# Kernel tuning notes

Hardware: AMD Instinct MI355X
Metric: run time of the kernel (lower is better)

Reference implementation:

```python
import jax, jax.numpy as jnp
import numpy as np

N = 50000   # atoms
E = 800000  # edges (avg degree 16)
F = 128     # n_atombasis
K = 64      # n_radialbasis
NRI = 3     # residual layers in interaction
NRA = 2     # atomic residual layers


def ssp(x):
    # PhysNet shifted softplus: softplus(x) - log(2)
    return jax.nn.softplus(x) - jnp.asarray(np.log(2.0), x.dtype)


def setup_inputs() -> dict:
    key = jax.random.key(0)
    ks = jax.random.split(key, 24)
    s = 0.05  # small weight scale (orig xavier gain=1e-4; nonzero so math is non-degenerate)
    inp = {
        "features": jax.random.normal(ks[0], (N, F), jnp.float32),
        "descriptors": jax.random.normal(ks[1], (E, K), jnp.float32),
        "idx_i": jnp.sort(jax.random.randint(ks[2], (E,), 0, N)),
        "idx_j": jax.random.randint(ks[3], (E,), 0, N),
        "Wdesc": jax.random.normal(ks[4], (F, K), jnp.float32) * s,   # desc2feat, no bias
        "Wi": jax.random.normal(ks[5], (F, F), jnp.float32) * s,
        "bi": jnp.zeros((F,), jnp.float32),
        "Wj": jax.random.normal(ks[6], (F, F), jnp.float32) * s,
        "bj": jnp.zeros((F,), jnp.float32),
        "Wri1": jax.random.normal(ks[7], (NRI, F, F), jnp.float32) * s,
        "bri1": jnp.zeros((NRI, F), jnp.float32),
        "Wri2": jax.random.normal(ks[8], (NRI, F, F), jnp.float32) * s,
        "bri2": jnp.zeros((NRI, F), jnp.float32),
        "Wd": jax.random.normal(ks[9], (F, F), jnp.float32) * s,
        "bd": jnp.zeros((F,), jnp.float32),
        "u": jnp.ones((F,), jnp.float32),
        "Wra1": jax.random.normal(ks[10], (NRA, F, F), jnp.float32) * s,
        "bra1": jnp.zeros((NRA, F), jnp.float32),
        "Wra2": jax.random.normal(ks[11], (NRA, F, F), jnp.float32) * s,
        "bra2": jnp.zeros((NRA, F), jnp.float32),
    }
    return inp


def _residual(m, W1, b1, W2, b2):
    # ResidualLayer (eval mode, no dropout): m + residual(dense(act(m)))
    y = ssp(m)
    h = ssp(y @ W1.T + b1)  # dense (with activation)
    return m + h @ W2.T + b2  # residual (no activation)


def reference(features, descriptors, Wdesc, Wi, bi, Wj, bj,
              Wri1, bri1, Wri2, bri2, Wd, bd, u,
              Wra1, bra1, Wra2, bra2, idx_i, idx_j):
    x = features                               # [N, F]
    xa = ssp(x)
    g = descriptors @ Wdesc.T                  # [E, F] edge gate
    xi = ssp(xa @ Wi.T + bi)                   # [N, F]
    xj_all = ssp(xa @ Wj.T + bj)               # [N, F]
    pxj = g * xj_all[idx_j]                    # gather -> elementwise mul, [E, F]
    xj = jax.ops.segment_sum(pxj, idx_i, num_segments=x.shape[0])  # scatter-add [N, F]
    message = xi + xj
    for k in range(NRI):
        message = _residual(message, Wri1[k], bri1[k], Wri2[k], bri2[k])
    message = ssp(message)
    x = u * x + message @ Wd.T + bd
    for k in range(NRA):
        x = _residual(x, Wra1[k], bra1[k], Wra2[k], bra2[k])
    return x
```

## Files before the change

### kernel.cpp

```cpp
#include <hip/hip_runtime.h>
#include <math.h>

#define NA 50000
#define NE 800000
#define FDIM 128
#define KDIM 64
#define NRI 3
#define NRA 2
#define ETILES 10

typedef unsigned short ushort_t;
typedef unsigned int uint_t;
typedef __attribute__((ext_vector_type(8))) short short8v;
typedef __attribute__((ext_vector_type(4))) float f32x4;
typedef __attribute__((ext_vector_type(4))) unsigned short u16x4;

__device__ __forceinline__ float ssp_f(float x) {
    float e = __expf(-fabsf(x));
    return fmaxf(x, 0.0f) + __logf(1.0f + e) - 0.69314718055994530942f;
}
__device__ __forceinline__ ushort_t f2bf(float x) {
    unsigned u = __float_as_uint(x);
    u += 0x7FFFu + ((u >> 16) & 1u);
    return (ushort_t)(u >> 16);
}
__device__ __forceinline__ float bf2f(ushort_t h) {
    return __uint_as_float(((unsigned)h) << 16);
}
__device__ __forceinline__ f32x4 ssp4(f32x4 v) {
    f32x4 r;
    #pragma unroll
    for (int j = 0; j < 4; ++j) r[j] = ssp_f(v[j]);
    return r;
}
__device__ __forceinline__ u16x4 pack4(f32x4 v) {
    u16x4 p;
    #pragma unroll
    for (int j = 0; j < 4; ++j) p[j] = f2bf(v[j]);
    return p;
}

__global__ __launch_bounds__(256) void k_wconv(
    const float* __restrict__ Wdesc, const float* __restrict__ Wi,
    const float* __restrict__ Wj,    const float* __restrict__ Wri1,
    const float* __restrict__ Wri2,  const float* __restrict__ Wd,
    const float* __restrict__ Wra1,  const float* __restrict__ Wra2,
    ushort_t* __restrict__ wbf)
{
    const int seg = blockIdx.y;
    const int idx = blockIdx.x * 2048 + threadIdx.x * 8;
    const float* s; ushort_t* d; int cnt;
    const int CH = 40960;
    switch (seg) {
    case 0: cnt = 8192;  if (idx >= cnt) return; s = Wdesc + idx; d = wbf + idx; break;
    case 1: cnt = 16384; if (idx >= cnt) return; s = Wi + idx;    d = wbf + 8192 + idx; break;
    case 2: cnt = 16384; if (idx >= cnt) return; s = Wj + idx;    d = wbf + 24576 + idx; break;
    case 3: { cnt = 3*16384; if (idx >= cnt) return; int k = idx/16384, o = idx - k*16384;
              s = Wri1 + idx; d = wbf + CH + (2*k)*16384 + o; break; }
    case 4: { cnt = 3*16384; if (idx >= cnt) return; int k = idx/16384, o = idx - k*16384;
              s = Wri2 + idx; d = wbf + CH + (2*k+1)*16384 + o; break; }
    case 5: cnt = 16384; if (idx >= cnt) return; s = Wd + idx; d = wbf + CH + 6*16384 + idx; break;
    case 6: { cnt = 2*16384; if (idx >= cnt) return; int k = idx/16384, o = idx - k*16384;
              s = Wra1 + idx; d = wbf + CH + (7+2*k)*16384 + o; break; }
    default:{ cnt = 2*16384; if (idx >= cnt) return; int k = idx/16384, o = idx - k*16384;
              s = Wra2 + idx; d = wbf + CH + (8+2*k)*16384 + o; break; }
    }
    #pragma unroll
    for (int j = 0; j < 8; ++j) d[j] = f2bf(s[j]);
}

__device__ __forceinline__ void stage_w(const ushort_t* __restrict__ src,
                                        ushort_t (*wlds)[136], int t)
{
    const int r = t >> 1, c0 = (t & 1) * 64;
    const short8v* s = (const short8v*)(src + (size_t)r * FDIM + c0);
    #pragma unroll
    for (int q = 0; q < 8; ++q)
        *(short8v*)&wlds[r][c0 + q * 8] = s[q];
}

__device__ __forceinline__ void gemm_tile_T(
    const ushort_t (*actA)[136], const ushort_t (*wlds)[136],
    int w, int lrow, int kgrp, const float* __restrict__ bias, f32x4 acc[8])
{
    short8v bfr[4];
    #pragma unroll
    for (int ks = 0; ks < 4; ++ks)
        bfr[ks] = *(const short8v*)&actA[16 * w + lrow][ks * 32 + kgrp * 8];
    #pragma unroll
    for (int nf = 0; nf < 8; ++nf)
        acc[nf] = *(const f32x4*)(bias + 16 * nf + 4 * kgrp);
    #pragma unroll
    for (int nf = 0; nf < 8; ++nf)
        #pragma unroll
        for (int ks = 0; ks < 4; ++ks) {
            short8v av = *(const short8v*)&wlds[16 * nf + lrow][ks * 32 + kgrp * 8];
            acc[nf] = __builtin_amdgcn_mfma_f32_16x16x32_bf16(av, bfr[ks], acc[nf], 0, 0, 0);
        }
}

__device__ __forceinline__ void write_act_T(
    ushort_t (*actA)[136], int w, int lrow, int kgrp, const f32x4 v[8])
{
    #pragma unroll
    for (int nf = 0; nf < 8; ++nf)
        *(u16x4*)&actA[16 * w + lrow][16 * nf + 4 * kgrp] = pack4(ssp4(v[nf]));
}

__global__ __launch_bounds__(256) void k_node_pre(
    const float* __restrict__ feat, const ushort_t* __restrict__ wbf,
    const float* __restrict__ bi, const float* __restrict__ bj,
    float* __restrict__ xi_out, ushort_t* __restrict__ xja_out)
{
    __shared__ ushort_t actA[64][136];
    __shared__ ushort_t wlds[128][136];
    const int t = threadIdx.x, lane = t & 63, w = t >> 6;
    const int lrow = lane & 15, kgrp = lane >> 4;
    const int atom = blockIdx.x * 64 + 16 * w + lrow;
    const bool ok = atom < NA;

    f32x4 v[8];
    #pragma unroll
    for (int nf = 0; nf < 8; ++nf)
        v[nf] = ok ? *(const f32x4*)(feat + (size_t)atom * FDIM + 16 * nf + 4 * kgrp)
                   : (f32x4){0.f, 0.f, 0.f, 0.f};
    write_act_T(actA, w, lrow, kgrp, v);
    __syncthreads();
    stage_w(wbf + 8192, wlds, t);
    __syncthreads();
    f32x4 acc[8];
    gemm_tile_T(actA, wlds, w, lrow, kgrp, bi, acc);
    if (ok)
        #pragma unroll
        for (int nf = 0; nf < 8; ++nf)
            *(f32x4*)(xi_out + (size_t)atom * FDIM + 16 * nf + 4 * kgrp) = ssp4(acc[nf]);
    __syncthreads();
    stage_w(wbf + 24576, wlds, t);
    __syncthreads();
    gemm_tile_T(actA, wlds, w, lrow, kgrp, bj, acc);
    if (ok)
        #pragma unroll
        for (int nf = 0; nf < 8; ++nf)
            *(u16x4*)(xja_out + (size_t)atom * FDIM + 16 * nf + 4 * kgrp) = pack4(ssp4(acc[nf]));
}

__device__ __forceinline__ short8v pack8(const float* p) {
    short8v r;
    #pragma unroll
    for (int j = 0; j < 8; ++j) r[j] = (short)f2bf(p[j]);
    return r;
}

__global__ __launch_bounds__(256) void k_edge_fused(
    const float* __restrict__ desc, const ushort_t* __restrict__ wdbf,
    const int* __restrict__ idx_i, const int* __restrict__ idx_j,
    const ushort_t* __restrict__ xja,
    float* __restrict__ msg)
{
    __shared__ ushort_t pl[64][136];
    __shared__ int ii[64];
    const int t = threadIdx.x, lane = t & 63, w = t >> 6;
    const int lrow = lane & 15, kgrp = lane >> 4;
    const int ebase = blockIdx.x * (64 * ETILES);
    const int eoff = w * 16 + lrow;

    short8v a[8][2];
    #pragma unroll
    for (int nf = 0; nf < 8; ++nf)
        #pragma unroll
        for (int ks = 0; ks < 2; ++ks)
            a[nf][ks] = *(const short8v*)(wdbf + (size_t)(16 * nf + lrow) * KDIM
                                          + ks * 32 + kgrp * 8);

    int er = ebase + eoff;
    int jj = idx_j[er];
    float t0[8], t1[8];
    {
        const float* q = desc + (size_t)er * KDIM + kgrp * 8;
        *(float4*)(t0)     = *(const float4*)q;
        *(float4*)(t0 + 4) = *(const float4*)(q + 4);
        *(float4*)(t1)     = *(const float4*)(q + 32);
        *(float4*)(t1 + 4) = *(const float4*)(q + 36);
    }

    for (int tt = 0; tt < ETILES; ++tt) {
        if (t < 64) ii[t] = idx_i[ebase + tt * 64 + t];

        short8v b0 = pack8(t0), b1 = pack8(t1);
        f32x4 acc[8];
        #pragma unroll
        for (int nf = 0; nf < 8; ++nf) acc[nf] = (f32x4){0.f, 0.f, 0.f, 0.f};
        #pragma unroll
        for (int nf = 0; nf < 8; ++nf) {
            acc[nf] = __builtin_amdgcn_mfma_f32_16x16x32_bf16(a[nf][0], b0, acc[nf], 0,0,0);
            acc[nf] = __builtin_amdgcn_mfma_f32_16x16x32_bf16(a[nf][1], b1, acc[nf], 0,0,0);
        }

        #pragma unroll
        for (int nf = 0; nf < 8; ++nf) {
            u16x4 xv = *(const u16x4*)(xja + (size_t)jj * FDIM + 16 * nf + 4 * kgrp);
            f32x4 pr;
            #pragma unroll
            for (int j = 0; j < 4; ++j) pr[j] = acc[nf][j] * bf2f(xv[j]);
            *(u16x4*)&pl[w * 16 + lrow][16 * nf + 4 * kgrp] = pack4(pr);
        }

        if (tt + 1 < ETILES) {
            er += 64;
            jj = idx_j[er];
            const float* q = desc + (size_t)er * KDIM + kgrp * 8;
            *(float4*)(t0)     = *(const float4*)q;
            *(float4*)(t0 + 4) = *(const float4*)(q + 4);
            *(float4*)(t1)     = *(const float4*)(q + 32);
            *(float4*)(t1 + 4) = *(const float4*)(q + 36);
        }

        __syncthreads();

        const int f = t & 127, h = t >> 7;
        const int r0 = h * 32;
        float s = 0.0f;
        int cur = ii[r0];
        #pragma unroll
        for (int g = 0; g < 8; ++g) {
            float v[4];
            int id[4];
            #pragma unroll
            for (int qq = 0; qq < 4; ++qq) {
                v[qq]  = bf2f(pl[r0 + g * 4 + qq][f]);
                id[qq] = ii[r0 + g * 4 + qq];
            }
            #pragma unroll
            for (int qq = 0; qq < 4; ++qq) {
                if (id[qq] != cur) {
                    unsafeAtomicAdd(&msg[(size_t)cur * FDIM + f], s);
                    s = 0.0f; cur = id[qq];
                }
                s += v[qq];
            }
        }
        unsafeAtomicAdd(&msg[(size_t)cur * FDIM + f], s);

        __syncthreads();
    }
}

__global__ __launch_bounds__(256) void k_chain(
    const float* __restrict__ msgp, const float* __restrict__ feat,
    const float* __restrict__ u, const ushort_t* __restrict__ wch,
    const float* __restrict__ bri1, const float* __restrict__ bri2,
    const float* __restrict__ bd,
    const float* __restrict__ bra1, const float* __restrict__ bra2,
    float* __restrict__ xout)
{
    __shared__ ushort_t actA[64][136];
    __shared__ ushort_t wlds[128][136];
    const int t = threadIdx.x, lane = t & 63, w = t >> 6;
    const int lrow = lane & 15, kgrp = lane >> 4;
    const int atom = blockIdx.x * 64 + 16 * w + lrow;
    const bool ok = atom < NA;

    f32x4 m[8], h[8], acc[8];
    #pragma unroll
    for (int nf = 0; nf < 8; ++nf)
        m[nf] = ok ? *(const f32x4*)(msgp + (size_t)atom * FDIM + 16 * nf + 4 * kgrp)
                   : (f32x4){0.f, 0.f, 0.f, 0.f};

    for (int k = 0; k < NRI; ++k) {
        write_act_T(actA, w, lrow, kgrp, m);
        __syncthreads();
        stage_w(wch + (size_t)(2 * k) * 16384, wlds, t);
        __syncthreads();
        gemm_tile_T(actA, wlds, w, lrow, kgrp, bri1 + k * FDIM, acc);
        #pragma unroll
        for (int nf = 0; nf < 8; ++nf) h[nf] = acc[nf];
        write_act_T(actA, w, lrow, kgrp, h);
        __syncthreads();
        stage_w(wch + (size_t)(2 * k + 1) * 16384, wlds, t);
        __syncthreads();
        gemm_tile_T(actA, wlds, w, lrow, kgrp, bri2 + k * FDIM, acc);
        #pragma unroll
        for (int nf = 0; nf < 8; ++nf) m[nf] += acc[nf];
    }

    write_act_T(actA, w, lrow, kgrp, m);
    __syncthreads();
    stage_w(wch + (size_t)6 * 16384, wlds, t);
    __syncthreads();
    gemm_tile_T(actA, wlds, w, lrow, kgrp, bd, acc);
    #pragma unroll
    for (int nf = 0; nf < 8; ++nf) {
        f32x4 fv = ok ? *(const f32x4*)(feat + (size_t)atom * FDIM + 16 * nf + 4 * kgrp)
                      : (f32x4){0.f, 0.f, 0.f, 0.f};
        f32x4 uv = *(const f32x4*)(u + 16 * nf + 4 * kgrp);
        m[nf] = uv * fv + acc[nf];
    }

    for (int k = 0; k < NRA; ++k) {
        write_act_T(actA, w, lrow, kgrp, m);
        __syncthreads();
        stage_w(wch + (size_t)(7 + 2 * k) * 16384, wlds, t);
        __syncthreads();
        gemm_tile_T(actA, wlds, w, lrow, kgrp, bra1 + k * FDIM, acc);
        #pragma unroll
        for (int nf = 0; nf < 8; ++nf) h[nf] = acc[nf];
        write_act_T(actA, w, lrow, kgrp, h);
        __syncthreads();
        stage_w(wch + (size_t)(8 + 2 * k) * 16384, wlds, t);
        __syncthreads();
        gemm_tile_T(actA, wlds, w, lrow, kgrp, bra2 + k * FDIM, acc);
        #pragma unroll
        for (int nf = 0; nf < 8; ++nf) m[nf] += acc[nf];
    }

    if (ok)
        #pragma unroll
        for (int nf = 0; nf < 8; ++nf)
            *(f32x4*)(xout + (size_t)atom * FDIM + 16 * nf + 4 * kgrp) = m[nf];
}

extern "C" void kernel_launch(void* const* d_in, const int* in_sizes, int n_in,
                              void* d_out, int out_size, void* d_ws, size_t ws_size,
                              hipStream_t stream)
{
    const float* feat  = (const float*)d_in[0];
    const float* desc  = (const float*)d_in[1];
    const int*   idx_i = (const int*)d_in[2];
    const int*   idx_j = (const int*)d_in[3];
    const float* Wdesc = (const float*)d_in[4];
    const float* Wi    = (const float*)d_in[5];
    const float* bi    = (const float*)d_in[6];
    const float* Wj    = (const float*)d_in[7];
    const float* bj    = (const float*)d_in[8];
    const float* Wri1  = (const float*)d_in[9];
    const float* bri1  = (const float*)d_in[10];
    const float* Wri2  = (const float*)d_in[11];
    const float* bri2  = (const float*)d_in[12];
    const float* Wd    = (const float*)d_in[13];
    const float* bd    = (const float*)d_in[14];
    const float* u     = (const float*)d_in[15];
    const float* Wra1  = (const float*)d_in[16];
    const float* bra1  = (const float*)d_in[17];
    const float* Wra2  = (const float*)d_in[18];
    const float* bra2  = (const float*)d_in[19];

    char* wsp = (char*)d_ws;
    float* msg = (float*)wsp;
    size_t off = (size_t)NA * FDIM * sizeof(float);
    ushort_t* xja = (ushort_t*)(wsp + off);
    off += (size_t)NA * FDIM * sizeof(ushort_t);
    ushort_t* wbf = (ushort_t*)(wsp + off);
    off += (((size_t)221184 * sizeof(ushort_t)) + 255) & ~(size_t)255;

    float* xout = (float*)d_out;
    const int nblk64 = (NA + 63) / 64;

    k_wconv<<<dim3(24, 8), 256, 0, stream>>>(Wdesc, Wi, Wj, Wri1, Wri2, Wd, Wra1, Wra2, wbf);
    k_node_pre<<<nblk64, 256, 0, stream>>>(feat, wbf, bi, bj, msg, xja);
    k_edge_fused<<<NE / (64 * ETILES), 256, 0, stream>>>(desc, wbf, idx_i, idx_j, xja, msg);
    k_chain<<<nblk64, 256, 0, stream>>>(msg, feat, u, wbf + 40960,
                                        bri1, bri2, bd, bra1, bra2, xout);
}
```

Measured before the change: 231.5 us.

## Double-buffer edge tile LDS, prefetch gathered xja rows, carry segment sums across tiles

The edge kernel now double-buffers the per-tile product and index arrays in shared memory, which removes the trailing barrier each tile needs. The gathered xja rows for the next tile are loaded ahead, alongside the descriptor prefetch, so the random-access gather latency overlaps the current tile's MFMA and reduction work. Running segment sums are carried across tiles and flushed only when the atom index changes, which cuts the number of atomic adds. The trade-off is more LDS per block and extra registers for the prefetched rows, which may lower occupancy.

```diff
diff --git a/kernel.cpp b/kernel.cpp
--- a/kernel.cpp
+++ b/kernel.cpp
@@ -157,8 +157,8 @@
     const ushort_t* __restrict__ xja,
     float* __restrict__ msg)
 {
-    __shared__ ushort_t pl[64][136];
-    __shared__ int ii[64];
+    __shared__ ushort_t pl[2][64][136];
+    __shared__ int ii[2][64];
     const int t = threadIdx.x, lane = t & 63, w = t >> 6;
     const int lrow = lane & 15, kgrp = lane >> 4;
     const int ebase = blockIdx.x * (64 * ETILES);
@@ -175,16 +175,26 @@
     int er = ebase + eoff;
     int jj = idx_j[er];
     float t0[8], t1[8];
+    u16x4 xv[8];
     {
         const float* q = desc + (size_t)er * KDIM + kgrp * 8;
         *(float4*)(t0)     = *(const float4*)q;
         *(float4*)(t0 + 4) = *(const float4*)(q + 4);
         *(float4*)(t1)     = *(const float4*)(q + 32);
         *(float4*)(t1 + 4) = *(const float4*)(q + 36);
-    }
+        #pragma unroll
+        for (int nf = 0; nf < 8; ++nf)
+            xv[nf] = *(const u16x4*)(xja + (size_t)jj * FDIM + 16 * nf + 4 * kgrp);
+    }
+
+    const int f = t & 127, h = t >> 7;
+    const int r0 = h * 32;
+    float s = 0.0f;
+    int cur = -1;
 
     for (int tt = 0; tt < ETILES; ++tt) {
-        if (t < 64) ii[t] = idx_i[ebase + tt * 64 + t];
+        const int buf = tt & 1;
+        if (t < 64) ii[buf][t] = idx_i[ebase + tt * 64 + t];
 
         short8v b0 = pack8(t0), b1 = pack8(t1);
         f32x4 acc[8];
@@ -198,11 +208,10 @@
 
         #pragma unroll
         for (int nf = 0; nf < 8; ++nf) {
-            u16x4 xv = *(const u16x4*)(xja + (size_t)jj * FDIM + 16 * nf + 4 * kgrp);
             f32x4 pr;
             #pragma unroll
-            for (int j = 0; j < 4; ++j) pr[j] = acc[nf][j] * bf2f(xv[j]);
-            *(u16x4*)&pl[w * 16 + lrow][16 * nf + 4 * kgrp] = pack4(pr);
+            for (int j = 0; j < 4; ++j) pr[j] = acc[nf][j] * bf2f(xv[nf][j]);
+            *(u16x4*)&pl[buf][w * 16 + lrow][16 * nf + 4 * kgrp] = pack4(pr);
         }
 
         if (tt + 1 < ETILES) {
@@ -213,36 +222,33 @@
             *(float4*)(t0 + 4) = *(const float4*)(q + 4);
             *(float4*)(t1)     = *(const float4*)(q + 32);
             *(float4*)(t1 + 4) = *(const float4*)(q + 36);
-        }
-
-        __syncthreads();
-
-        const int f = t & 127, h = t >> 7;
-        const int r0 = h * 32;
-        float s = 0.0f;
-        int cur = ii[r0];
+            #pragma unroll
+            for (int nf = 0; nf < 8; ++nf)
+                xv[nf] = *(const u16x4*)(xja + (size_t)jj * FDIM + 16 * nf + 4 * kgrp);
+        }
+
+        __syncthreads();
+
         #pragma unroll
         for (int g = 0; g < 8; ++g) {
             float v[4];
             int id[4];
             #pragma unroll
             for (int qq = 0; qq < 4; ++qq) {
-                v[qq]  = bf2f(pl[r0 + g * 4 + qq][f]);
-                id[qq] = ii[r0 + g * 4 + qq];
+                v[qq]  = bf2f(pl[buf][r0 + g * 4 + qq][f]);
+                id[qq] = ii[buf][r0 + g * 4 + qq];
             }
             #pragma unroll
             for (int qq = 0; qq < 4; ++qq) {
                 if (id[qq] != cur) {
-                    unsafeAtomicAdd(&msg[(size_t)cur * FDIM + f], s);
+                    if (cur >= 0) unsafeAtomicAdd(&msg[(size_t)cur * FDIM + f], s);
                     s = 0.0f; cur = id[qq];
                 }
                 s += v[qq];
             }
         }
-        unsafeAtomicAdd(&msg[(size_t)cur * FDIM + f], s);
-
-        __syncthreads();
-    }
+    }
+    if (cur >= 0) unsafeAtomicAdd(&msg[(size_t)cur * FDIM + f], s);
 }
 
 __global__ __launch_bounds__(256) void k_chain(
```

Measured after the change: 226.4 us (median of 2 runs). -2.2%, faster.
